# Kernel optimization log

Hardware: AMD Instinct MI355X
Metric: run time of the kernel (lower is better)

The kernel has to match this reference:

```python
import jax, jax.numpy as jnp
import numpy as np

CK = 64  # key channels, used for the 1/sqrt(ck) scale


def setup_inputs() -> dict:
    key = jax.random.key(0)
    ks = jax.random.split(key, 9)
    B, C, D, H, W = 2, 64, 20, 20, 20
    ck = cv = co = 64
    s = 0.02
    return {
        "x": jax.random.normal(ks[0], (B, C, D, H, W), dtype=jnp.float32),
        "wq": jax.random.normal(ks[1], (ck, C), dtype=jnp.float32) * s,
        "bq": jax.random.normal(ks[2], (ck,), dtype=jnp.float32) * s,
        "wk": jax.random.normal(ks[3], (ck, C), dtype=jnp.float32) * s,
        "bk": jax.random.normal(ks[4], (ck,), dtype=jnp.float32) * s,
        "wv": jax.random.normal(ks[5], (cv, C), dtype=jnp.float32) * s,
        "bv": jax.random.normal(ks[6], (cv,), dtype=jnp.float32) * s,
        "wo": jax.random.normal(ks[7], (co, cv), dtype=jnp.float32) * s,
        "bo": jax.random.normal(ks[8], (co,), dtype=jnp.float32) * s,
    }


def reference(x, wq, bq, wk, bk, wv, bv, wo, bo):
    B, C, D, H, W = x.shape
    ck = wq.shape[0]
    cv = wv.shape[0]
    xf = x.reshape(B, C, -1)  # (B, C, N) with N = D*H*W
    # 1x1x1 convs == per-voxel channel matmuls
    q = jnp.einsum('kc,bcn->bnk', wq, xf) + bq           # (B, N, ck) queries (already transposed)
    k = jnp.einsum('kc,bcn->bkn', wk, xf) + bk[:, None]  # (B, ck, N) keys
    v = jnp.einsum('vc,bcn->bnv', wv, xf) + bv           # (B, N, cv) values (transposed)
    scale = 1.0 / jnp.sqrt(jnp.asarray(CK, dtype=x.dtype))
    attn = jax.nn.softmax(jnp.einsum('bnk,bkm->bnm', q, k) * scale, axis=-1)  # (B, N, N)
    # dropout is identity in eval mode
    out = jnp.einsum('bnm,bmv->bnv', attn, v)  # (B, N, cv)
    # faithful to torch: .view(batch, cv, d, h, w) reinterprets memory, no transpose
    out = out.reshape(B, cv, D, H, W)
    out = jnp.einsum('oc,bcdhw->bodhw', wo, out) + bo[None, :, None, None, None]
    return out
```

## Files before the change

### kernel.cpp

```cpp
#include <hip/hip_runtime.h>
#include <hip/hip_bf16.h>

typedef __bf16 bf16_t;
typedef __bf16 bf16x8 __attribute__((ext_vector_type(8)));
typedef float f32x4 __attribute__((ext_vector_type(4)));

#define NV 8000
#define QB 125

__device__ __forceinline__ bf16x8 cvt_bf16x8(const float* __restrict__ p) {
    float4 a = *reinterpret_cast<const float4*>(p);
    float4 b = *reinterpret_cast<const float4*>(p + 4);
    bf16x8 r;
    r[0] = (bf16_t)a.x; r[1] = (bf16_t)a.y; r[2] = (bf16_t)a.z; r[3] = (bf16_t)a.w;
    r[4] = (bf16_t)b.x; r[5] = (bf16_t)b.y; r[6] = (bf16_t)b.z; r[7] = (bf16_t)b.w;
    return r;
}

__device__ __forceinline__ unsigned pack2(float a, float b) {
    union { bf16_t h[2]; unsigned u; } x;
    x.h[0] = (bf16_t)a; x.h[1] = (bf16_t)b;
    return x.u;
}

__device__ __forceinline__ int sigma_of(int n) {
    int c = n / 125, a = n - 125 * c;
    return a * 64 + c;
}

__global__ __launch_bounds__(256) void qkv_kernel(
    const float* __restrict__ x,
    const float* __restrict__ wq, const float* __restrict__ bq,
    const float* __restrict__ wk, const float* __restrict__ bk,
    const float* __restrict__ wv, const float* __restrict__ bv,
    bf16_t* __restrict__ Q, bf16_t* __restrict__ Kr, bf16_t* __restrict__ Vt)
{
    __shared__ __align__(16) char xb[16 * 128];

    const int tid = threadIdx.x;
    const int b  = blockIdx.x / 500;
    const int n0 = (blockIdx.x % 500) * 16;

    {
        int c = tid >> 2, seg = tid & 3;
        float4 v4 = *reinterpret_cast<const float4*>(&x[((size_t)b * 64 + c) * NV + n0 + seg * 4]);
        #pragma unroll
        for (int j = 0; j < 4; ++j) {
            int vx = seg * 4 + j;
            *reinterpret_cast<bf16_t*>(xb + vx * 128 + ((c * 2) ^ ((vx & 7) << 4))) =
                (bf16_t)((&v4.x)[j]);
        }
    }
    __syncthreads();

    const int w  = tid >> 6;
    const int lane = tid & 63;
    const int g  = lane >> 4;
    const int lr = lane & 15;

    const bf16x8 xa0 = *reinterpret_cast<const bf16x8*>(
        xb + lr * 128 + ((16 * g) ^ ((lr & 7) << 4)));
    const bf16x8 xa1 = *reinterpret_cast<const bf16x8*>(
        xb + lr * 128 + ((64 + 16 * g) ^ ((lr & 7) << 4)));

    const f32x4 zero4 = {0.f, 0.f, 0.f, 0.f};
    const float QSCALE = 0.125f * 1.44269504088896f;
    const int kout = w * 16 + lr;

    {
        bf16x8 wb0 = cvt_bf16x8(wq + kout * 64 + 8 * g);
        bf16x8 wb1 = cvt_bf16x8(wq + kout * 64 + 32 + 8 * g);
        f32x4 acc = __builtin_amdgcn_mfma_f32_16x16x32_bf16(xa0, wb0, zero4, 0, 0, 0);
        acc = __builtin_amdgcn_mfma_f32_16x16x32_bf16(xa1, wb1, acc, 0, 0, 0);
        const float bias = bq[kout];
        #pragma unroll
        for (int j = 0; j < 4; ++j) {
            const int sig = sigma_of(n0 + 4 * g + j);
            Q[((size_t)b * NV + sig) * 64 + kout] = (bf16_t)((acc[j] + bias) * QSCALE);
        }
    }
    {
        bf16x8 wb0 = cvt_bf16x8(wk + kout * 64 + 8 * g);
        bf16x8 wb1 = cvt_bf16x8(wk + kout * 64 + 32 + 8 * g);
        f32x4 acc = __builtin_amdgcn_mfma_f32_16x16x32_bf16(xa0, wb0, zero4, 0, 0, 0);
        acc = __builtin_amdgcn_mfma_f32_16x16x32_bf16(xa1, wb1, acc, 0, 0, 0);
        const float bias = bk[kout];
        #pragma unroll
        for (int j = 0; j < 4; ++j)
            Kr[((size_t)b * NV + n0 + 4 * g + j) * 64 + kout] = (bf16_t)(acc[j] + bias);
    }
    {
        bf16x8 wb0 = cvt_bf16x8(wv + kout * 64 + 8 * g);
        bf16x8 wb1 = cvt_bf16x8(wv + kout * 64 + 32 + 8 * g);
        f32x4 acc = __builtin_amdgcn_mfma_f32_16x16x32_bf16(xa0, wb0, zero4, 0, 0, 0);
        acc = __builtin_amdgcn_mfma_f32_16x16x32_bf16(xa1, wb1, acc, 0, 0, 0);
        const float bias = bv[kout];
        union { uint2 u2; bf16_t h[4]; } pk;
        #pragma unroll
        for (int j = 0; j < 4; ++j) pk.h[j] = (bf16_t)(acc[j] + bias);
        *reinterpret_cast<uint2*>(&Vt[((size_t)b * 64 + kout) * NV + n0 + 4 * g]) = pk.u2;
    }
}

template<int S>
__global__ __launch_bounds__(256) void attn_kernel(
    const bf16_t* __restrict__ Q, const bf16_t* __restrict__ Kr,
    const bf16_t* __restrict__ Vt, float* __restrict__ Op, float* __restrict__ ml)
{
    __shared__ __align__(16) char kt[64 * 128];
    __shared__ __align__(16) char vt[64 * 128];
    __shared__ __align__(16) char pt[4 * 2048];

    const int tid  = threadIdx.x;
    const int s    = blockIdx.x % S;
    const int rem  = blockIdx.x / S;
    const int b    = rem / QB;
    const int q0   = (rem % QB) * 64;
    const int t0   = (125 * s) / S;
    const int t1   = (125 * (s + 1)) / S;
    const int w    = tid >> 6;
    const int lane = tid & 63;
    const int g    = lane >> 4;
    const int lr   = lane & 15;

    bf16x8 qa0, qa1;
    {
        const size_t qbase = ((size_t)b * NV + q0 + w * 16 + lr) * 64;
        qa0 = *reinterpret_cast<const bf16x8*>(&Q[qbase + 8 * g]);
        qa1 = *reinterpret_cast<const bf16x8*>(&Q[qbase + 32 + 8 * g]);
    }

    const int srow = tid >> 3;
    const int sch  = tid & 7;
    const int dst0 = srow * 128 + ((sch * 16) ^ ((srow & 7) << 4));
    const int dst1 = (srow + 32) * 128 + ((sch * 16) ^ ((srow & 7) << 4));
    const bf16_t* kp = Kr + (size_t)b * NV * 64;
    const bf16_t* vp = Vt + (size_t)b * 64 * NV;

    uint4 rk0, rk1, rv0, rv1;
    {
        const int m0 = t0 * 64;
        rk0 = *reinterpret_cast<const uint4*>(&kp[(size_t)(m0 + srow) * 64 + sch * 8]);
        rk1 = *reinterpret_cast<const uint4*>(&kp[(size_t)(m0 + srow + 32) * 64 + sch * 8]);
        rv0 = *reinterpret_cast<const uint4*>(&vp[(size_t)srow * NV + m0 + sch * 8]);
        rv1 = *reinterpret_cast<const uint4*>(&vp[(size_t)(srow + 32) * NV + m0 + sch * 8]);
    }

    const f32x4 zero4 = {0.f, 0.f, 0.f, 0.f};
    f32x4 oacc[4];
    float m = -1e30f, l = 0.f;
    #pragma unroll
    for (int vf = 0; vf < 4; ++vf) oacc[vf] = zero4;

    char* ptw = pt + w * 2048 + lr * 128;
    const int xsw = (lr & 7) << 2;

    for (int t = t0; t < t1; ++t) {
        __syncthreads();
        *reinterpret_cast<uint4*>(kt + dst0) = rk0;
        *reinterpret_cast<uint4*>(kt + dst1) = rk1;
        *reinterpret_cast<uint4*>(vt + dst0) = rv0;
        *reinterpret_cast<uint4*>(vt + dst1) = rv1;
        __syncthreads();

        const int tn = (t + 1 < t1) ? t + 1 : t;
        const int mn0 = tn * 64;
        uint4 nk0 = *reinterpret_cast<const uint4*>(&kp[(size_t)(mn0 + srow) * 64 + sch * 8]);
        uint4 nk1 = *reinterpret_cast<const uint4*>(&kp[(size_t)(mn0 + srow + 32) * 64 + sch * 8]);
        uint4 nv0 = *reinterpret_cast<const uint4*>(&vp[(size_t)srow * NV + mn0 + sch * 8]);
        uint4 nv1 = *reinterpret_cast<const uint4*>(&vp[(size_t)(srow + 32) * NV + mn0 + sch * 8]);

        f32x4 sf[4];
        #pragma unroll
        for (int cf = 0; cf < 4; ++cf) {
            const int row  = cf * 16 + lr;
            const int roff = row * 128;
            const int swz  = (row & 7) << 4;
            const bf16x8 kb0 = *reinterpret_cast<const bf16x8*>(kt + roff + ((16 * g) ^ swz));
            const bf16x8 kb1 = *reinterpret_cast<const bf16x8*>(kt + roff + ((64 + 16 * g) ^ swz));
            sf[cf] = __builtin_amdgcn_mfma_f32_16x16x32_bf16(kb0, qa0, zero4, 0, 0, 0);
            sf[cf] = __builtin_amdgcn_mfma_f32_16x16x32_bf16(kb1, qa1, sf[cf], 0, 0, 0);
        }

        float mx;
        {
            f32x4 t01 = sf[0], t23 = sf[2];
            #pragma unroll
            for (int j = 0; j < 4; ++j) {
                t01[j] = fmaxf(sf[0][j], sf[1][j]);
                t23[j] = fmaxf(sf[2][j], sf[3][j]);
            }
            float a0 = fmaxf(fmaxf(t01[0], t01[1]), fmaxf(t01[2], t01[3]));
            float a1 = fmaxf(fmaxf(t23[0], t23[1]), fmaxf(t23[2], t23[3]));
            mx = fmaxf(a0, a1);
        }
        mx = fmaxf(mx, __shfl_xor(mx, 16, 64));
        mx = fmaxf(mx, __shfl_xor(mx, 32, 64));

        if (__any(mx > m + 8.0f)) {
            const float mn2 = fmaxf(m, mx);
            const float corr = exp2f(m - mn2);
            m = mn2;
            l *= corr;
            #pragma unroll
            for (int vf = 0; vf < 4; ++vf) oacc[vf] *= corr;
        }

        float ps = 0.f;
        #pragma unroll
        for (int cf = 0; cf < 4; ++cf) {
            float p0 = exp2f(sf[cf][0] - m);
            float p1 = exp2f(sf[cf][1] - m);
            float p2 = exp2f(sf[cf][2] - m);
            float p3 = exp2f(sf[cf][3] - m);
            ps += (p0 + p1) + (p2 + p3);
            uint2 pw;
            pw.x = pack2(p0, p1);
            pw.y = pack2(p2, p3);
            const int slot = (8 * cf + 2 * g) ^ xsw;
            *reinterpret_cast<uint2*>(ptw + slot * 4) = pw;
        }
        ps += __shfl_xor(ps, 16, 64);
        ps += __shfl_xor(ps, 32, 64);
        l += ps;

        #pragma unroll
        for (int ms = 0; ms < 2; ++ms) {
            union { uint4 u; bf16x8 v; } pf;
            pf.u = *reinterpret_cast<const uint4*>(ptw + (((16 * ms + 4 * g) ^ xsw) * 4));
            #pragma unroll
            for (int vf = 0; vf < 4; ++vf) {
                const int vrow = vf * 16 + lr;
                const bf16x8 vb = *reinterpret_cast<const bf16x8*>(
                    vt + vrow * 128 + ((ms * 64 + 16 * g) ^ ((vrow & 7) << 4)));
                oacc[vf] = __builtin_amdgcn_mfma_f32_16x16x32_bf16(vb, pf.v, oacc[vf], 0, 0, 0);
            }
        }

        rk0 = nk0; rk1 = nk1; rv0 = nv0; rv1 = nv1;
    }

    const size_t obase = (size_t)(s * 2 + b) * NV;
    const int qrow = q0 + w * 16 + lr;
    #pragma unroll
    for (int vf = 0; vf < 4; ++vf) {
        *reinterpret_cast<f32x4*>(&Op[(obase + qrow) * 64 + vf * 16 + 4 * g]) = oacc[vf];
    }
    if (g == 0) {
        float2 t2; t2.x = m; t2.y = l;
        *reinterpret_cast<float2*>(&ml[(obase + qrow) * 2]) = t2;
    }
}

template<int S>
__global__ __launch_bounds__(256) void projc_kernel(
    const float* __restrict__ Op, const float* __restrict__ ml,
    const float* __restrict__ wo, const float* __restrict__ bo,
    float* __restrict__ out)
{
    __shared__ __align__(16) char bt[64 * 128];
    __shared__ float al[64 * 8];

    const int tid = threadIdx.x;
    const int b   = blockIdx.x / 125;
    const int a   = blockIdx.x % 125;

    if (tid < 64) {
        const int row = a * 64 + tid;
        float M = -1e30f;
        #pragma unroll
        for (int s = 0; s < S; ++s)
            M = fmaxf(M, ml[((size_t)(s * 2 + b) * NV + row) * 2]);
        float L = 0.f, av[S];
        #pragma unroll
        for (int s = 0; s < S; ++s) {
            const float mm = ml[((size_t)(s * 2 + b) * NV + row) * 2];
            const float ll = ml[((size_t)(s * 2 + b) * NV + row) * 2 + 1];
            const float aa = exp2f(mm - M);
            L += ll * aa;
            av[s] = aa;
        }
        const float inv = 1.0f / L;
        #pragma unroll
        for (int s = 0; s < S; ++s) al[tid * 8 + s] = av[s] * inv;
    }
    __syncthreads();

    {
        const int c = tid >> 2, sg = tid & 3;
        f32x4 acc[4] = {{0,0,0,0},{0,0,0,0},{0,0,0,0},{0,0,0,0}};
        #pragma unroll
        for (int s = 0; s < S; ++s) {
            const float fac = al[c * 8 + s];
            const float* base = &Op[((size_t)(s * 2 + b) * NV + a * 64 + c) * 64 + sg * 16];
            #pragma unroll
            for (int q = 0; q < 4; ++q)
                acc[q] += fac * *reinterpret_cast<const f32x4*>(base + q * 4);
        }
        #pragma unroll
        for (int q = 0; q < 4; ++q) {
            #pragma unroll
            for (int j = 0; j < 4; ++j) {
                const int v = sg * 16 + q * 4 + j;
                *reinterpret_cast<bf16_t*>(bt + v * 128 + ((c * 2) ^ ((v & 7) << 4))) =
                    (bf16_t)acc[q][j];
            }
        }
    }
    __syncthreads();

    const int w  = tid >> 6;
    const int lane = tid & 63;
    const int g  = lane >> 4;
    const int lr = lane & 15;

    const int orow = w * 16 + lr;
    const bf16x8 wa0 = cvt_bf16x8(wo + orow * 64 + 8 * g);
    const bf16x8 wa1 = cvt_bf16x8(wo + orow * 64 + 32 + 8 * g);
    const float4 bo4 = *reinterpret_cast<const float4*>(&bo[w * 16 + 4 * g]);

    const f32x4 zero4 = {0.f, 0.f, 0.f, 0.f};
    #pragma unroll
    for (int nf = 0; nf < 4; ++nf) {
        const int rrow = nf * 16 + lr;
        const bf16x8 gb0 = *reinterpret_cast<const bf16x8*>(
            bt + rrow * 128 + ((16 * g) ^ ((rrow & 7) << 4)));
        const bf16x8 gb1 = *reinterpret_cast<const bf16x8*>(
            bt + rrow * 128 + ((64 + 16 * g) ^ ((rrow & 7) << 4)));
        f32x4 acc = __builtin_amdgcn_mfma_f32_16x16x32_bf16(wa0, gb0, zero4, 0, 0, 0);
        acc = __builtin_amdgcn_mfma_f32_16x16x32_bf16(wa1, gb1, acc, 0, 0, 0);
        #pragma unroll
        for (int j = 0; j < 4; ++j) {
            const int o = w * 16 + 4 * g + j;
            out[((size_t)b * 64 + o) * NV + a * 64 + nf * 16 + lr] = acc[j] + (&bo4.x)[j];
        }
    }
}

extern "C" void kernel_launch(void* const* d_in, const int* in_sizes, int n_in,
                              void* d_out, int out_size, void* d_ws, size_t ws_size,
                              hipStream_t stream)
{
    const float* x  = (const float*)d_in[0];
    const float* wq = (const float*)d_in[1];
    const float* bq = (const float*)d_in[2];
    const float* wk = (const float*)d_in[3];
    const float* bk = (const float*)d_in[4];
    const float* wv = (const float*)d_in[5];
    const float* bv = (const float*)d_in[6];
    const float* wo = (const float*)d_in[7];
    const float* bo = (const float*)d_in[8];
    float* out = (float*)d_out;

    char* ws = (char*)d_ws;
    bf16_t* Q  = (bf16_t*)(ws);
    bf16_t* Kr = (bf16_t*)(ws + 2048000);
    bf16_t* Vt = (bf16_t*)(ws + 4096000);

    int S = 4;
    if (ws_size < 6144000ull + 4ull * 4224000ull) S = 2;
    if (ws_size < 6144000ull + 2ull * 4224000ull) S = 1;

    float* Op = (float*)(ws + 6144000);
    float* ml = (float*)(ws + 6144000 + (size_t)S * 4096000);

    qkv_kernel<<<dim3(2 * 500), dim3(256), 0, stream>>>(x, wq, bq, wk, bk, wv, bv, Q, Kr, Vt);

    if (S == 4) {
        attn_kernel<4><<<dim3(4 * 2 * QB), dim3(256), 0, stream>>>(Q, Kr, Vt, Op, ml);
        projc_kernel<4><<<dim3(2 * 125), dim3(256), 0, stream>>>(Op, ml, wo, bo, out);
    } else if (S == 2) {
        attn_kernel<2><<<dim3(2 * 2 * QB), dim3(256), 0, stream>>>(Q, Kr, Vt, Op, ml);
        projc_kernel<2><<<dim3(2 * 125), dim3(256), 0, stream>>>(Op, ml, wo, bo, out);
    } else {
        attn_kernel<1><<<dim3(1 * 2 * QB), dim3(256), 0, stream>>>(Q, Kr, Vt, Op, ml);
        projc_kernel<1><<<dim3(2 * 125), dim3(256), 0, stream>>>(Op, ml, wo, bo, out);
    }
}
```

Baseline: 165.3 us.

## Use 32x32 MFMA with 128-query tiles, async LDS double-buffering, and 8-way KV split

Rewrites the attention kernel to use 32x32x16 bf16 MFMA tiles, with each wave handling 32 queries so a block covers 128 queries. K/V tiles are now loaded with global_load_lds directly into double-buffered shared memory instead of being staged through registers, which removes one barrier per iteration. The KV split factor goes up to 8 when the workspace allows it, keeping the grid large despite the bigger query tiles. The last query tile is padded by clamping the row index, which costs some wasted work and more partial-result traffic into the combine kernel.

```diff
diff --git a/kernel.cpp b/kernel.cpp
--- a/kernel.cpp
+++ b/kernel.cpp
@@ -4,9 +4,14 @@
 typedef __bf16 bf16_t;
 typedef __bf16 bf16x8 __attribute__((ext_vector_type(8)));
 typedef float f32x4 __attribute__((ext_vector_type(4)));
+typedef float f32x16 __attribute__((ext_vector_type(16)));
 
 #define NV 8000
 #define QB 125
+
+#define GLOAD_LDS16(src, dst) \
+    __builtin_amdgcn_global_load_lds((const __attribute__((address_space(1))) void*)(src), \
+                                     (__attribute__((address_space(3))) void*)(dst), 16, 0, 0)
 
 __device__ __forceinline__ bf16x8 cvt_bf16x8(const float* __restrict__ p) {
     float4 a = *reinterpret_cast<const float4*>(p);
@@ -107,94 +112,93 @@
     const bf16_t* __restrict__ Q, const bf16_t* __restrict__ Kr,
     const bf16_t* __restrict__ Vt, float* __restrict__ Op, float* __restrict__ ml)
 {
-    __shared__ __align__(16) char kt[64 * 128];
-    __shared__ __align__(16) char vt[64 * 128];
-    __shared__ __align__(16) char pt[4 * 2048];
+    __shared__ __align__(16) char kt[2][8192];
+    __shared__ __align__(16) char vt[2][8192];
+    __shared__ __align__(16) char pt[4][4096];
 
     const int tid  = threadIdx.x;
     const int s    = blockIdx.x % S;
     const int rem  = blockIdx.x / S;
-    const int b    = rem / QB;
-    const int q0   = (rem % QB) * 64;
+    const int b    = rem / 63;
+    const int qb   = rem % 63;
+    const int q0   = qb * 128;
     const int t0   = (125 * s) / S;
     const int t1   = (125 * (s + 1)) / S;
     const int w    = tid >> 6;
     const int lane = tid & 63;
-    const int g    = lane >> 4;
-    const int lr   = lane & 15;
-
-    bf16x8 qa0, qa1;
-    {
-        const size_t qbase = ((size_t)b * NV + q0 + w * 16 + lr) * 64;
-        qa0 = *reinterpret_cast<const bf16x8*>(&Q[qbase + 8 * g]);
-        qa1 = *reinterpret_cast<const bf16x8*>(&Q[qbase + 32 + 8 * g]);
-    }
-
-    const int srow = tid >> 3;
-    const int sch  = tid & 7;
-    const int dst0 = srow * 128 + ((sch * 16) ^ ((srow & 7) << 4));
-    const int dst1 = (srow + 32) * 128 + ((sch * 16) ^ ((srow & 7) << 4));
-    const bf16_t* kp = Kr + (size_t)b * NV * 64;
-    const bf16_t* vp = Vt + (size_t)b * 64 * NV;
-
-    uint4 rk0, rk1, rv0, rv1;
+    const int lo   = lane & 31;
+    const int hi   = lane >> 5;
+
+    const int q  = q0 + w * 32 + lo;
+    const int qc = q < NV ? q : NV - 1;
+
+    bf16x8 bq[4];
+    {
+        const bf16_t* qrow = Q + ((size_t)b * NV + qc) * 64 + hi * 8;
+        #pragma unroll
+        for (int kk = 0; kk < 4; ++kk)
+            bq[kk] = *reinterpret_cast<const bf16x8*>(qrow + kk * 16);
+    }
+
+    const char* kp = (const char*)(Kr + (size_t)b * NV * 64);
+    const char* vp = (const char*)(Vt + (size_t)b * 64 * NV);
+
+    const int srr = lane >> 3;
+    const int sch = lane & 7;
+
+    f32x16 acco[2]; acco[0] = f32x16{}; acco[1] = f32x16{};
+    float m = -1e30f, l = 0.f;
+
+    char* ptw = &pt[w][0] + lo * 128;
+    const int swzq = (lo & 7) << 4;
+
     {
         const int m0 = t0 * 64;
-        rk0 = *reinterpret_cast<const uint4*>(&kp[(size_t)(m0 + srow) * 64 + sch * 8]);
-        rk1 = *reinterpret_cast<const uint4*>(&kp[(size_t)(m0 + srow + 32) * 64 + sch * 8]);
-        rv0 = *reinterpret_cast<const uint4*>(&vp[(size_t)srow * NV + m0 + sch * 8]);
-        rv1 = *reinterpret_cast<const uint4*>(&vp[(size_t)(srow + 32) * NV + m0 + sch * 8]);
-    }
-
-    const f32x4 zero4 = {0.f, 0.f, 0.f, 0.f};
-    f32x4 oacc[4];
-    float m = -1e30f, l = 0.f;
-    #pragma unroll
-    for (int vf = 0; vf < 4; ++vf) oacc[vf] = zero4;
-
-    char* ptw = pt + w * 2048 + lr * 128;
-    const int xsw = (lr & 7) << 2;
+        #pragma unroll
+        for (int rnd = 0; rnd < 2; ++rnd) {
+            const int r = w * 16 + rnd * 8 + srr;
+            const int cb = (sch * 16) ^ ((r & 7) << 4);
+            GLOAD_LDS16(kp + (size_t)(m0 + r) * 128 + cb, kt[0] + w * 2048 + rnd * 1024);
+            GLOAD_LDS16(vp + (size_t)r * (NV * 2) + m0 * 2 + cb, vt[0] + w * 2048 + rnd * 1024);
+        }
+    }
 
     for (int t = t0; t < t1; ++t) {
+        const int cur = (t - t0) & 1;
         __syncthreads();
-        *reinterpret_cast<uint4*>(kt + dst0) = rk0;
-        *reinterpret_cast<uint4*>(kt + dst1) = rk1;
-        *reinterpret_cast<uint4*>(vt + dst0) = rv0;
-        *reinterpret_cast<uint4*>(vt + dst1) = rv1;
-        __syncthreads();
-
-        const int tn = (t + 1 < t1) ? t + 1 : t;
-        const int mn0 = tn * 64;
-        uint4 nk0 = *reinterpret_cast<const uint4*>(&kp[(size_t)(mn0 + srow) * 64 + sch * 8]);
-        uint4 nk1 = *reinterpret_cast<const uint4*>(&kp[(size_t)(mn0 + srow + 32) * 64 + sch * 8]);
-        uint4 nv0 = *reinterpret_cast<const uint4*>(&vp[(size_t)srow * NV + mn0 + sch * 8]);
-        uint4 nv1 = *reinterpret_cast<const uint4*>(&vp[(size_t)(srow + 32) * NV + mn0 + sch * 8]);
-
-        f32x4 sf[4];
-        #pragma unroll
-        for (int cf = 0; cf < 4; ++cf) {
-            const int row  = cf * 16 + lr;
-            const int roff = row * 128;
-            const int swz  = (row & 7) << 4;
-            const bf16x8 kb0 = *reinterpret_cast<const bf16x8*>(kt + roff + ((16 * g) ^ swz));
-            const bf16x8 kb1 = *reinterpret_cast<const bf16x8*>(kt + roff + ((64 + 16 * g) ^ swz));
-            sf[cf] = __builtin_amdgcn_mfma_f32_16x16x32_bf16(kb0, qa0, zero4, 0, 0, 0);
-            sf[cf] = __builtin_amdgcn_mfma_f32_16x16x32_bf16(kb1, qa1, sf[cf], 0, 0, 0);
-        }
-
-        float mx;
-        {
-            f32x4 t01 = sf[0], t23 = sf[2];
-            #pragma unroll
-            for (int j = 0; j < 4; ++j) {
-                t01[j] = fmaxf(sf[0][j], sf[1][j]);
-                t23[j] = fmaxf(sf[2][j], sf[3][j]);
-            }
-            float a0 = fmaxf(fmaxf(t01[0], t01[1]), fmaxf(t01[2], t01[3]));
-            float a1 = fmaxf(fmaxf(t23[0], t23[1]), fmaxf(t23[2], t23[3]));
-            mx = fmaxf(a0, a1);
-        }
-        mx = fmaxf(mx, __shfl_xor(mx, 16, 64));
+        if (t + 1 < t1) {
+            const int m0n = (t + 1) * 64;
+            #pragma unroll
+            for (int rnd = 0; rnd < 2; ++rnd) {
+                const int r = w * 16 + rnd * 8 + srr;
+                const int cb = (sch * 16) ^ ((r & 7) << 4);
+                GLOAD_LDS16(kp + (size_t)(m0n + r) * 128 + cb, kt[cur ^ 1] + w * 2048 + rnd * 1024);
+                GLOAD_LDS16(vp + (size_t)r * (NV * 2) + m0n * 2 + cb, vt[cur ^ 1] + w * 2048 + rnd * 1024);
+            }
+        }
+
+        const char* ktb = kt[cur];
+        f32x16 sa[2];
+        #pragma unroll
+        for (int kb = 0; kb < 2; ++kb) {
+            const int krow = kb * 32 + lo;
+            const int roff = krow * 128;
+            const int swzk = (krow & 7) << 4;
+            f32x16 acc{};
+            #pragma unroll
+            for (int kk = 0; kk < 4; ++kk) {
+                const bf16x8 ka = *reinterpret_cast<const bf16x8*>(
+                    ktb + roff + ((kk * 32 + hi * 16) ^ swzk));
+                acc = __builtin_amdgcn_mfma_f32_32x32x16_bf16(ka, bq[kk], acc, 0, 0, 0);
+            }
+            sa[kb] = acc;
+        }
+
+        float mx = sa[0][0];
+        #pragma unroll
+        for (int r = 1; r < 16; ++r) mx = fmaxf(mx, sa[0][r]);
+        #pragma unroll
+        for (int r = 0; r < 16; ++r) mx = fmaxf(mx, sa[1][r]);
         mx = fmaxf(mx, __shfl_xor(mx, 32, 64));
 
         if (__any(mx > m + 8.0f)) {
@@ -202,53 +206,59 @@
             const float corr = exp2f(m - mn2);
             m = mn2;
             l *= corr;
-            #pragma unroll
-            for (int vf = 0; vf < 4; ++vf) oacc[vf] *= corr;
+            acco[0] *= corr;
+            acco[1] *= corr;
         }
 
         float ps = 0.f;
         #pragma unroll
-        for (int cf = 0; cf < 4; ++cf) {
-            float p0 = exp2f(sf[cf][0] - m);
-            float p1 = exp2f(sf[cf][1] - m);
-            float p2 = exp2f(sf[cf][2] - m);
-            float p3 = exp2f(sf[cf][3] - m);
-            ps += (p0 + p1) + (p2 + p3);
-            uint2 pw;
-            pw.x = pack2(p0, p1);
-            pw.y = pack2(p2, p3);
-            const int slot = (8 * cf + 2 * g) ^ xsw;
-            *reinterpret_cast<uint2*>(ptw + slot * 4) = pw;
-        }
-        ps += __shfl_xor(ps, 16, 64);
+        for (int kb = 0; kb < 2; ++kb) {
+            #pragma unroll
+            for (int j = 0; j < 4; ++j) {
+                float p0 = exp2f(sa[kb][4 * j + 0] - m);
+                float p1 = exp2f(sa[kb][4 * j + 1] - m);
+                float p2 = exp2f(sa[kb][4 * j + 2] - m);
+                float p3 = exp2f(sa[kb][4 * j + 3] - m);
+                ps += (p0 + p1) + (p2 + p3);
+                uint2 pw;
+                pw.x = pack2(p0, p1);
+                pw.y = pack2(p2, p3);
+                *reinterpret_cast<uint2*>(ptw + ((64 * kb + 16 * j + 8 * hi) ^ swzq)) = pw;
+            }
+        }
         ps += __shfl_xor(ps, 32, 64);
         l += ps;
 
-        #pragma unroll
-        for (int ms = 0; ms < 2; ++ms) {
+        const char* vtb = vt[cur];
+        #pragma unroll
+        for (int ks = 0; ks < 4; ++ks) {
             union { uint4 u; bf16x8 v; } pf;
-            pf.u = *reinterpret_cast<const uint4*>(ptw + (((16 * ms + 4 * g) ^ xsw) * 4));
-            #pragma unroll
-            for (int vf = 0; vf < 4; ++vf) {
-                const int vrow = vf * 16 + lr;
-                const bf16x8 vb = *reinterpret_cast<const bf16x8*>(
-                    vt + vrow * 128 + ((ms * 64 + 16 * g) ^ ((vrow & 7) << 4)));
-                oacc[vf] = __builtin_amdgcn_mfma_f32_16x16x32_bf16(vb, pf.v, oacc[vf], 0, 0, 0);
-            }
-        }
-
-        rk0 = nk0; rk1 = nk1; rv0 = nv0; rv1 = nv1;
-    }
-
-    const size_t obase = (size_t)(s * 2 + b) * NV;
-    const int qrow = q0 + w * 16 + lr;
-    #pragma unroll
-    for (int vf = 0; vf < 4; ++vf) {
-        *reinterpret_cast<f32x4*>(&Op[(obase + qrow) * 64 + vf * 16 + 4 * g]) = oacc[vf];
-    }
-    if (g == 0) {
-        float2 t2; t2.x = m; t2.y = l;
-        *reinterpret_cast<float2*>(&ml[(obase + qrow) * 2]) = t2;
+            pf.u = *reinterpret_cast<const uint4*>(ptw + ((ks * 32 + hi * 16) ^ swzq));
+            #pragma unroll
+            for (int vb = 0; vb < 2; ++vb) {
+                const int vrow = vb * 32 + lo;
+                const bf16x8 va = *reinterpret_cast<const bf16x8*>(
+                    vtb + vrow * 128 + ((ks * 32 + hi * 16) ^ ((vrow & 7) << 4)));
+                acco[vb] = __builtin_amdgcn_mfma_f32_32x32x16_bf16(va, pf.v, acco[vb], 0, 0, 0);
+            }
+        }
+    }
+
+    if (q < NV) {
+        const size_t obase = ((size_t)(s * 2 + b) * NV + q) * 64;
+        #pragma unroll
+        for (int vb = 0; vb < 2; ++vb) {
+            #pragma unroll
+            for (int j = 0; j < 4; ++j) {
+                f32x4 o4 = { acco[vb][4 * j + 0], acco[vb][4 * j + 1],
+                             acco[vb][4 * j + 2], acco[vb][4 * j + 3] };
+                *reinterpret_cast<f32x4*>(&Op[obase + vb * 32 + 8 * j + 4 * hi]) = o4;
+            }
+        }
+        if (hi == 0) {
+            float2 t2; t2.x = m; t2.y = l;
+            *reinterpret_cast<float2*>(&ml[((size_t)(s * 2 + b) * NV + q) * 2]) = t2;
+        }
     }
 }
 
@@ -294,16 +304,16 @@
             const float fac = al[c * 8 + s];
             const float* base = &Op[((size_t)(s * 2 + b) * NV + a * 64 + c) * 64 + sg * 16];
             #pragma unroll
-            for (int q = 0; q < 4; ++q)
-                acc[q] += fac * *reinterpret_cast<const f32x4*>(base + q * 4);
-        }
-        #pragma unroll
-        for (int q = 0; q < 4; ++q) {
+            for (int qq = 0; qq < 4; ++qq)
+                acc[qq] += fac * *reinterpret_cast<const f32x4*>(base + qq * 4);
+        }
+        #pragma unroll
+        for (int qq = 0; qq < 4; ++qq) {
             #pragma unroll
             for (int j = 0; j < 4; ++j) {
-                const int v = sg * 16 + q * 4 + j;
+                const int v = sg * 16 + qq * 4 + j;
                 *reinterpret_cast<bf16_t*>(bt + v * 128 + ((c * 2) ^ ((v & 7) << 4))) =
-                    (bf16_t)acc[q][j];
+                    (bf16_t)acc[qq][j];
             }
         }
     }
@@ -357,7 +367,8 @@
     bf16_t* Kr = (bf16_t*)(ws + 2048000);
     bf16_t* Vt = (bf16_t*)(ws + 4096000);
 
-    int S = 4;
+    int S = 8;
+    if (ws_size < 6144000ull + 8ull * 4224000ull) S = 4;
     if (ws_size < 6144000ull + 4ull * 4224000ull) S = 2;
     if (ws_size < 6144000ull + 2ull * 4224000ull) S = 1;
 
@@ -366,14 +377,17 @@
 
     qkv_kernel<<<dim3(2 * 500), dim3(256), 0, stream>>>(x, wq, bq, wk, bk, wv, bv, Q, Kr, Vt);
 
-    if (S == 4) {
-        attn_kernel<4><<<dim3(4 * 2 * QB), dim3(256), 0, stream>>>(Q, Kr, Vt, Op, ml);
+    if (S == 8) {
+        attn_kernel<8><<<dim3(8 * 2 * 63), dim3(256), 0, stream>>>(Q, Kr, Vt, Op, ml);
+        projc_kernel<8><<<dim3(2 * 125), dim3(256), 0, stream>>>(Op, ml, wo, bo, out);
+    } else if (S == 4) {
+        attn_kernel<4><<<dim3(4 * 2 * 63), dim3(256), 0, stream>>>(Q, Kr, Vt, Op, ml);
         projc_kernel<4><<<dim3(2 * 125), dim3(256), 0, stream>>>(Op, ml, wo, bo, out);
     } else if (S == 2) {
-        attn_kernel<2><<<dim3(2 * 2 * QB), dim3(256), 0, stream>>>(Q, Kr, Vt, Op, ml);
+        attn_kernel<2><<<dim3(2 * 2 * 63), dim3(256), 0, stream>>>(Q, Kr, Vt, Op, ml);
         projc_kernel<2><<<dim3(2 * 125), dim3(256), 0, stream>>>(Op, ml, wo, bo, out);
     } else {
-        attn_kernel<1><<<dim3(1 * 2 * QB), dim3(256), 0, stream>>>(Q, Kr, Vt, Op, ml);
+        attn_kernel<1><<<dim3(1 * 2 * 63), dim3(256), 0, stream>>>(Q, Kr, Vt, Op, ml);
         projc_kernel<1><<<dim3(2 * 125), dim3(256), 0, stream>>>(Op, ml, wo, bo, out);
     }
 }
```

Result: slower. 170.7 us (+3.3%).
